# Performance work log

Measured on AMD Instinct MI355X. Metric: run time of the kernel, lower is better.

Reference implementation:

```python
import jax, jax.numpy as jnp
import numpy as np
from functools import partial

D = 1024
H = 4 * D
E = 8
K_TOP = 2
B, T = 4, 2048
NEG_INF = jnp.float32(-1e30)


def setup_inputs() -> dict:
    key = jax.random.key(0)
    ks = jax.random.split(key, 12)
    s = 0.02
    return {
        "x": jax.random.normal(ks[0], (B, T, D), jnp.float32),
        "noise": jax.random.normal(ks[1], (B, T, E), jnp.float32),
        "gate_w": jax.random.normal(ks[2], (E, D), jnp.float32) * s,
        "gate_b": jnp.zeros((E,), jnp.float32),
        "var_w": jax.random.normal(ks[3], (E, D), jnp.float32) * s,
        "var_b": jnp.zeros((E,), jnp.float32),
        "w1": jax.random.normal(ks[4], (E, H, D), jnp.float32) * s,
        "b1": jnp.zeros((E, H), jnp.float32),
        "w2": jax.random.normal(ks[5], (E, D, H), jnp.float32) * s,
        "b2": jnp.zeros((E, D), jnp.float32),
    }


def reference(x, noise, gate_w, gate_b, var_w, var_b, w1, b1, w2, b2):
    # Noisy top-k gating
    logits = jnp.einsum("btd,ed->bte", x, gate_w) + gate_b          # [B,T,E]
    std = jax.nn.softplus(jnp.einsum("btd,ed->bte", x, var_w) + var_b)
    noisy = logits + noise * std                                      # [B,T,E]
    _, idx = jax.lax.top_k(noisy, K_TOP)                              # [B,T,K]
    # boolean top-k mask over experts
    mask = (idx[..., None] == jnp.arange(E)).any(axis=-2)             # [B,T,E]
    coef = jax.nn.softmax(jnp.where(mask, noisy, NEG_INF), axis=-1)   # zeros outside top-k

    # Combine: sum_e coef_e * FFN_e(x). coef is exactly 0 for non-selected
    # experts, so this equals the masked gather/scatter math. Scan over the
    # small expert dim to avoid a [E,B,T,H] intermediate.
    coef_e = jnp.moveaxis(coef, -1, 0)                                # [E,B,T]

    def body(acc, ew):
        w1e, b1e, w2e, b2e, ce = ew
        h = jax.nn.relu(jnp.einsum("btd,hd->bth", x, w1e) + b1e)
        y = jnp.einsum("bth,dh->btd", h, w2e) + b2e
        return acc + y * ce[..., None], None

    out, _ = jax.lax.scan(body, jnp.zeros_like(x), (w1, b1, w2, b2, coef_e))
    return out
```

## Files before the change

### kernel.cpp

```cpp
#include <hip/hip_runtime.h>
#include <hip/hip_bf16.h>
#include <math.h>

#define NTOK 8192
#define DD   1024
#define HH   4096
#define NE   8
#define BM 256
#define BN 256
#define BK 64
#define SLOT_CAP (2 * NTOK + NE * BM)

typedef __bf16 bf16;
typedef __bf16 bf16x8 __attribute__((ext_vector_type(8)));
typedef __bf16 bf16x4 __attribute__((ext_vector_type(4)));
typedef float  f32x4  __attribute__((ext_vector_type(4)));

typedef __attribute__((address_space(3))) unsigned char lds_u8;
typedef const __attribute__((address_space(1))) unsigned char g_u8;

__device__ __forceinline__ void gload16(const bf16* g, bf16* l) {
  __builtin_amdgcn_global_load_lds((g_u8*)g, (lds_u8*)l, 16, 0, 0);
}

__device__ __forceinline__ float softplus_f(float v) {
  return fmaxf(v, 0.f) + log1pf(expf(-fabsf(v)));
}

__global__ __launch_bounds__(64) void moe_gate_kernel(
    const float* __restrict__ x, const float* __restrict__ noise,
    const float* __restrict__ gate_w, const float* __restrict__ gate_b,
    const float* __restrict__ var_w,  const float* __restrict__ var_b,
    float* __restrict__ coef2, int* __restrict__ t2e, int* __restrict__ counts)
{
  const int t = blockIdx.x;
  const int lane = threadIdx.x;
  const float* xt = x + (size_t)t * DD;
  float pg[NE], pv[NE];
  #pragma unroll
  for (int e = 0; e < NE; ++e) { pg[e] = 0.f; pv[e] = 0.f; }
  #pragma unroll 4
  for (int i = 0; i < DD / 64; ++i) {
    const int d = lane + i * 64;
    const float xv = xt[d];
    #pragma unroll
    for (int e = 0; e < NE; ++e) {
      pg[e] = fmaf(xv, gate_w[e * DD + d], pg[e]);
      pv[e] = fmaf(xv, var_w[e * DD + d], pv[e]);
    }
  }
  #pragma unroll
  for (int e = 0; e < NE; ++e) {
    #pragma unroll
    for (int off = 32; off; off >>= 1) {
      pg[e] += __shfl_xor(pg[e], off);
      pv[e] += __shfl_xor(pv[e], off);
    }
  }
  if (lane == 0) {
    float noisy[NE];
    #pragma unroll
    for (int e = 0; e < NE; ++e) {
      const float lg = pg[e] + gate_b[e];
      const float sd = softplus_f(pv[e] + var_b[e]);
      noisy[e] = lg + noise[t * NE + e] * sd;
    }
    int i1 = 0; float n1 = noisy[0];
    #pragma unroll
    for (int e = 1; e < NE; ++e) if (noisy[e] > n1) { n1 = noisy[e]; i1 = e; }
    int i2 = -1; float n2 = -3.0e38f;
    #pragma unroll
    for (int e = 0; e < NE; ++e) if (e != i1 && noisy[e] > n2) { n2 = noisy[e]; i2 = e; }
    const float e2 = expf(n2 - n1);
    const float den = 1.f + e2;
    coef2[t * 2 + 0] = 1.f / den;
    coef2[t * 2 + 1] = e2 / den;
    t2e[t * 2 + 0] = i1;
    t2e[t * 2 + 1] = i2;
    atomicAdd(&counts[i1], 1);
    atomicAdd(&counts[i2], 1);
  }
}

__global__ void moe_offsets_kernel(const int* __restrict__ counts, int* __restrict__ po) {
  if (threadIdx.x == 0) {
    int acc = 0;
    po[0] = 0;
    for (int e = 0; e < NE; ++e) {
      acc += ((counts[e] + BM - 1) / BM) * BM;
      po[e + 1] = acc;
    }
  }
}

__global__ __launch_bounds__(256) void moe_scatter_kernel(
    const int* __restrict__ t2e, const float* __restrict__ coef2,
    const int* __restrict__ po, int* __restrict__ cnt2,
    int* __restrict__ assign_tok, float* __restrict__ slot_coef)
{
  const int t = blockIdx.x * 256 + threadIdx.x;
  if (t >= NTOK) return;
  #pragma unroll
  for (int k = 0; k < 2; ++k) {
    const int e = t2e[t * 2 + k];
    const int pos = atomicAdd(&cnt2[e], 1);
    const int slot = po[e] + pos;
    assign_tok[slot] = t;
    slot_coef[slot] = coef2[t * 2 + k];
  }
}

__global__ __launch_bounds__(256) void cvt_bf16_kernel(const float* __restrict__ src,
                                                       bf16* __restrict__ dst, int n4) {
  for (int i = blockIdx.x * 256 + threadIdx.x; i < n4; i += gridDim.x * 256) {
    const float4 f = ((const float4*)src)[i];
    bf16x4 v;
    v[0] = (bf16)f.x; v[1] = (bf16)f.y; v[2] = (bf16)f.z; v[3] = (bf16)f.w;
    ((bf16x4*)dst)[i] = v;
  }
}

template<int KDIM, int NCOLS, bool FFN1>
__global__ __launch_bounds__(512, 2) void moe_gemm_kernel(
    const bf16* __restrict__ Asrc, const bf16* __restrict__ Wsrc,
    const float* __restrict__ bias,
    const int* __restrict__ assign_tok, const float* __restrict__ slot_coef,
    const int* __restrict__ po,
    bf16* __restrict__ hout, float* __restrict__ out,
    int chunk_base, int gx)
{
  __shared__ bf16 smA[2][BM * BK];
  __shared__ bf16 smB[2][BN * BK];
  __shared__ int toks[BM];

  const int nwg = gx * (NCOLS / BN);
  const int lin = blockIdx.x;
  const int q = nwg >> 3, r = nwg & 7;
  const int xcd = lin & 7, idx = lin >> 3;
  const int wg = (xcd < r ? xcd * (q + 1) : r * (q + 1) + (xcd - r) * q) + idx;
  const int bx = wg % gx, by = wg / gx;

  const int row0 = chunk_base + bx * BM;
  const int po8 = po[NE];
  if (row0 >= po8) return;
  int e = 0;
  while (row0 >= po[e + 1]) ++e;
  const int bn0 = by * BN;
  const bf16* We = Wsrc + (size_t)e * ((size_t)HH * DD);

  const int tid = threadIdx.x, lane = tid & 63;
  if (tid < BM) toks[tid] = assign_tok[row0 + tid];
  __syncthreads();

  const int t7 = tid & 7;
  const bf16* aptr[4];
  const bf16* bptr[4];
  #pragma unroll
  for (int i = 0; i < 4; ++i) {
    const int g = i * 512 + tid;
    const int row = g >> 3;
    const int c8 = ((t7 ^ (row & 7)) * 8);
    int ar;
    if constexpr (FFN1) {
      const int s = toks[row];
      ar = s < 0 ? 0 : s;
    } else {
      ar = row0 - chunk_base + row;
    }
    aptr[i] = Asrc + (size_t)ar * KDIM + c8;
    bptr[i] = We + (size_t)(bn0 + row) * KDIM + c8;
  }

  auto stage = [&](int sel, int k0) {
    #pragma unroll
    for (int i = 0; i < 4; ++i)
      gload16(aptr[i] + k0, &smA[sel][(i * 512 + tid) * 8]);
    #pragma unroll
    for (int i = 0; i < 4; ++i)
      gload16(bptr[i] + k0, &smB[sel][(i * 512 + tid) * 8]);
  };

  const int wid = tid >> 6, wr = wid >> 2, wc = wid & 3;
  const int la = lane & 15, hi = lane >> 4;
  f32x4 acc[8][4];
  #pragma unroll
  for (int m = 0; m < 8; ++m)
    #pragma unroll
    for (int n = 0; n < 4; ++n) acc[m][n] = {0.f, 0.f, 0.f, 0.f};

  constexpr int NK = KDIM / BK;
  stage(0, 0);
  __syncthreads();
  #pragma unroll 2
  for (int ks = 0; ks < NK; ++ks) {
    const int cur = ks & 1;
    if (ks + 1 < NK) stage(cur ^ 1, (ks + 1) * BK);
    const bf16* A = smA[cur];
    const bf16* B = smB[cur];
    #pragma unroll
    for (int kk = 0; kk < 2; ++kk) {
      bf16x8 af[8], bf_[4];
      #pragma unroll
      for (int m = 0; m < 8; ++m) {
        const int rw = wr * 128 + m * 16 + la;
        const int c8 = ((kk * 4 + hi) ^ (rw & 7)) * 8;
        af[m] = *(const bf16x8*)(A + rw * 64 + c8);
      }
      #pragma unroll
      for (int n = 0; n < 4; ++n) {
        const int rw = wc * 64 + n * 16 + la;
        const int c8 = ((kk * 4 + hi) ^ (rw & 7)) * 8;
        bf_[n] = *(const bf16x8*)(B + rw * 64 + c8);
      }
      #pragma unroll
      for (int m = 0; m < 8; ++m)
        #pragma unroll
        for (int n = 0; n < 4; ++n)
          acc[m][n] = __builtin_amdgcn_mfma_f32_16x16x32_bf16(af[m], bf_[n], acc[m][n], 0, 0, 0);
    }
    __syncthreads();
  }

  if constexpr (FFN1) {
    #pragma unroll
    for (int n = 0; n < 4; ++n) {
      const int col = bn0 + wc * 64 + n * 16 + la;
      const float bb = bias[e * NCOLS + col];
      #pragma unroll
      for (int m = 0; m < 8; ++m) {
        const int rl = wr * 128 + m * 16 + hi * 4;
        #pragma unroll
        for (int rr = 0; rr < 4; ++rr) {
          float v = acc[m][n][rr] + bb;
          v = v > 0.f ? v : 0.f;
          hout[(size_t)(row0 - chunk_base + rl + rr) * HH + col] = (bf16)v;
        }
      }
    }
  } else {
    #pragma unroll
    for (int n = 0; n < 4; ++n) {
      const int col = bn0 + wc * 64 + n * 16 + la;
      const float bb = bias[e * NCOLS + col];
      #pragma unroll
      for (int m = 0; m < 8; ++m) {
        const int rl = wr * 128 + m * 16 + hi * 4;
        #pragma unroll
        for (int rr = 0; rr < 4; ++rr) {
          const int tl = rl + rr;
          const int tok = toks[tl];
          if (tok >= 0) {
            const float c = slot_coef[row0 + tl];
            atomicAdd(out + (size_t)tok * DD + col, c * (acc[m][n][rr] + bb));
          }
        }
      }
    }
  }
}

extern "C" void kernel_launch(void* const* d_in, const int* in_sizes, int n_in,
                              void* d_out, int out_size, void* d_ws, size_t ws_size,
                              hipStream_t stream) {
  const float* x      = (const float*)d_in[0];
  const float* noise  = (const float*)d_in[1];
  const float* gate_w = (const float*)d_in[2];
  const float* gate_b = (const float*)d_in[3];
  const float* var_w  = (const float*)d_in[4];
  const float* var_b  = (const float*)d_in[5];
  const float* w1     = (const float*)d_in[6];
  const float* b1     = (const float*)d_in[7];
  const float* w2     = (const float*)d_in[8];
  const float* b2     = (const float*)d_in[9];
  float* out = (float*)d_out;
  (void)in_sizes; (void)n_in; (void)out_size;

  char* ws = (char*)d_ws;
  size_t off = 0;
  auto alloc = [&](size_t bytes) {
    off = (off + 255) & ~(size_t)255;
    size_t o = off;
    off += bytes;
    return o;
  };
  bf16*  xb         = (bf16*)(ws + alloc((size_t)NTOK * DD * 2));
  float* coef2      = (float*)(ws + alloc((size_t)NTOK * 2 * 4));
  int*   t2e        = (int*)(ws + alloc((size_t)NTOK * 2 * 4));
  int*   counts     = (int*)(ws + alloc(64));
  int*   cnt2       = counts + 8;
  int*   po         = (int*)(ws + alloc(64));
  int*   assign_tok = (int*)(ws + alloc((size_t)SLOT_CAP * 4));
  float* slot_coef  = (float*)(ws + alloc((size_t)SLOT_CAP * 4));
  bf16*  w1b        = (bf16*)(ws + alloc((size_t)NE * HH * DD * 2));
  bf16*  w2b        = (bf16*)(ws + alloc((size_t)NE * DD * HH * 2));
  off = (off + 255) & ~(size_t)255;
  const size_t h_avail = ws_size > off ? ws_size - off : 0;
  int chunk_rows = (int)(h_avail / ((size_t)HH * 2));
  chunk_rows = (chunk_rows / BM) * BM;
  if (chunk_rows < BM) chunk_rows = BM;
  if (chunk_rows > SLOT_CAP) chunk_rows = SLOT_CAP;
  bf16* hbuf = (bf16*)(ws + off);

  hipMemsetAsync(counts, 0, 64, stream);
  hipMemsetAsync(assign_tok, 0xFF, (size_t)SLOT_CAP * 4, stream);
  hipMemsetAsync(out, 0, (size_t)NTOK * DD * 4, stream);

  moe_gate_kernel<<<NTOK, 64, 0, stream>>>(x, noise, gate_w, gate_b, var_w, var_b,
                                           coef2, t2e, counts);
  moe_offsets_kernel<<<1, 64, 0, stream>>>(counts, po);
  moe_scatter_kernel<<<NTOK / 256, 256, 0, stream>>>(t2e, coef2, po, cnt2,
                                                     assign_tok, slot_coef);
  cvt_bf16_kernel<<<2048, 256, 0, stream>>>(x, xb, NTOK * DD / 4);
  cvt_bf16_kernel<<<2048, 256, 0, stream>>>(w1, w1b, NE * HH * DD / 4);
  cvt_bf16_kernel<<<2048, 256, 0, stream>>>(w2, w2b, NE * DD * HH / 4);

  const int rounds = (SLOT_CAP + chunk_rows - 1) / chunk_rows;
  for (int r = 0; r < rounds; ++r) {
    const int cb = r * chunk_rows;
    const int rows_here = (cb + chunk_rows <= SLOT_CAP) ? chunk_rows : (SLOT_CAP - cb);
    const int gx = rows_here / BM;
    moe_gemm_kernel<DD, HH, true><<<gx * (HH / BN), 512, 0, stream>>>(
        xb, w1b, b1, assign_tok, slot_coef, po, hbuf, nullptr, cb, gx);
    moe_gemm_kernel<HH, DD, false><<<gx * (DD / BN), 512, 0, stream>>>(
        hbuf, w2b, b2, assign_tok, slot_coef, po, nullptr, out, cb, gx);
  }
}
```

Baseline: 995.0 us.

## Rewrite MoE GEMM mainloop with 4-stage LDS pipeline and split-K FFN2

Replaces the double-buffered BK=64 mainloop with a four-deep ring of BK=32 stages, using manual vmcnt waits and raw barriers so global-to-LDS loads overlap MFMA work. MFMA bursts are wrapped in setprio, and A fragments are loaded in two halves to reduce register pressure. The second FFN GEMM is split along K into two z-slices that accumulate atomically, with only slice zero adding bias, to put more workgroups on the device. The change adds deeper pipelining and a new LDS swizzle, and doubles the atomic traffic on the output.

```diff
diff --git a/kernel.cpp b/kernel.cpp
--- a/kernel.cpp
+++ b/kernel.cpp
@@ -8,7 +8,6 @@
 #define NE   8
 #define BM 256
 #define BN 256
-#define BK 64
 #define SLOT_CAP (2 * NTOK + NE * BM)
 
 typedef __bf16 bf16;
@@ -120,8 +119,8 @@
   }
 }
 
-template<int KDIM, int NCOLS, bool FFN1>
-__global__ __launch_bounds__(512, 2) void moe_gemm_kernel(
+template<int KDIM, int KSTRIDE, int NCOLS, bool FFN1>
+__global__ __launch_bounds__(512, 2) void moe_gemm8_kernel(
     const bf16* __restrict__ Asrc, const bf16* __restrict__ Wsrc,
     const float* __restrict__ bias,
     const int* __restrict__ assign_tok, const float* __restrict__ slot_coef,
@@ -129,8 +128,10 @@
     bf16* __restrict__ hout, float* __restrict__ out,
     int chunk_base, int gx)
 {
-  __shared__ bf16 smA[2][BM * BK];
-  __shared__ bf16 smB[2][BN * BK];
+  constexpr int NI  = KDIM / 128;
+  constexpr int KHT = KDIM / 32;
+  __shared__ bf16 smA[32768];
+  __shared__ bf16 smB[32768];
   __shared__ int toks[BM];
 
   const int nwg = gx * (NCOLS / BN);
@@ -146,82 +147,88 @@
   int e = 0;
   while (row0 >= po[e + 1]) ++e;
   const int bn0 = by * BN;
-  const bf16* We = Wsrc + (size_t)e * ((size_t)HH * DD);
-
-  const int tid = threadIdx.x, lane = tid & 63;
+  const size_t kbase = (size_t)blockIdx.z * KDIM;
+  const bf16* We = Wsrc + (size_t)e * ((size_t)HH * DD) + kbase;
+  const bf16* As = Asrc + kbase;
+
+  const int tid = threadIdx.x, lane = tid & 63, wid = tid >> 6;
   if (tid < BM) toks[tid] = assign_tok[row0 + tid];
   __syncthreads();
 
-  const int t7 = tid & 7;
-  const bf16* aptr[4];
-  const bf16* bptr[4];
-  #pragma unroll
-  for (int i = 0; i < 4; ++i) {
-    const int g = i * 512 + tid;
-    const int row = g >> 3;
-    const int c8 = ((t7 ^ (row & 7)) * 8);
-    int ar;
-    if constexpr (FFN1) {
-      const int s = toks[row];
-      ar = s < 0 ? 0 : s;
-    } else {
-      ar = row0 - chunk_base + row;
-    }
-    aptr[i] = Asrc + (size_t)ar * KDIM + c8;
-    bptr[i] = We + (size_t)(bn0 + row) * KDIM + c8;
-  }
-
-  auto stage = [&](int sel, int k0) {
-    #pragma unroll
-    for (int i = 0; i < 4; ++i)
-      gload16(aptr[i] + k0, &smA[sel][(i * 512 + tid) * 8]);
-    #pragma unroll
-    for (int i = 0; i < 4; ++i)
-      gload16(bptr[i] + k0, &smB[sel][(i * 512 + tid) * 8]);
+  const int srcc = (((lane & 3) ^ ((lane >> 2) & 3)) * 8);
+  const int rt0 = wid * 16 + (lane >> 2);
+  const int rt1 = (8 + wid) * 16 + (lane >> 2);
+  int ar0, ar1;
+  if constexpr (FFN1) {
+    const int s0 = toks[rt0]; ar0 = s0 < 0 ? 0 : s0;
+    const int s1 = toks[rt1]; ar1 = s1 < 0 ? 0 : s1;
+  } else {
+    ar0 = row0 - chunk_base + rt0;
+    ar1 = row0 - chunk_base + rt1;
+  }
+  const bf16* ap0 = As + (size_t)ar0 * KSTRIDE + srcc;
+  const bf16* ap1 = As + (size_t)ar1 * KSTRIDE + srcc;
+  const bf16* bp0 = We + (size_t)(bn0 + rt0) * KSTRIDE + srcc;
+  const bf16* bp1 = We + (size_t)(bn0 + rt1) * KSTRIDE + srcc;
+
+  auto stage = [&](int rr, int kh) {
+    const int ko = kh * 32;
+    gload16(ap0 + ko, &smA[rr * 8192 + wid * 512]);
+    gload16(ap1 + ko, &smA[rr * 8192 + (8 + wid) * 512]);
+    gload16(bp0 + ko, &smB[rr * 8192 + wid * 512]);
+    gload16(bp1 + ko, &smB[rr * 8192 + (8 + wid) * 512]);
   };
 
-  const int wid = tid >> 6, wr = wid >> 2, wc = wid & 3;
+  const int wr = wid >> 2, wc = wid & 3;
   const int la = lane & 15, hi = lane >> 4;
+  const int cph = (hi ^ (la & 3)) * 8;
+  const int aBase = wr * 4096 + la * 32 + cph;
+  const int bBase = wc * 2048 + la * 32 + cph;
+
   f32x4 acc[8][4];
   #pragma unroll
   for (int m = 0; m < 8; ++m)
     #pragma unroll
     for (int n = 0; n < 4; ++n) acc[m][n] = {0.f, 0.f, 0.f, 0.f};
 
-  constexpr int NK = KDIM / BK;
-  stage(0, 0);
-  __syncthreads();
-  #pragma unroll 2
-  for (int ks = 0; ks < NK; ++ks) {
-    const int cur = ks & 1;
-    if (ks + 1 < NK) stage(cur ^ 1, (ks + 1) * BK);
-    const bf16* A = smA[cur];
-    const bf16* B = smB[cur];
-    #pragma unroll
-    for (int kk = 0; kk < 2; ++kk) {
-      bf16x8 af[8], bf_[4];
-      #pragma unroll
-      for (int m = 0; m < 8; ++m) {
-        const int rw = wr * 128 + m * 16 + la;
-        const int c8 = ((kk * 4 + hi) ^ (rw & 7)) * 8;
-        af[m] = *(const bf16x8*)(A + rw * 64 + c8);
-      }
-      #pragma unroll
-      for (int n = 0; n < 4; ++n) {
-        const int rw = wc * 64 + n * 16 + la;
-        const int c8 = ((kk * 4 + hi) ^ (rw & 7)) * 8;
-        bf_[n] = *(const bf16x8*)(B + rw * 64 + c8);
-      }
-      #pragma unroll
-      for (int m = 0; m < 8; ++m)
+  stage(0, 0); stage(1, 1); stage(2, 2);
+
+  for (int i = 0; i < NI; ++i) {
+    #pragma unroll
+    for (int pp = 0; pp < 4; ++pp) {
+      asm volatile("s_waitcnt vmcnt(8)" ::: "memory");
+      asm volatile("s_barrier" ::: "memory");
+      bf16x8 a0[4], bb[4];
+      #pragma unroll
+      for (int m = 0; m < 4; ++m)
+        a0[m] = *(const bf16x8*)(&smA[pp * 8192 + aBase + m * 512]);
+      #pragma unroll
+      for (int n = 0; n < 4; ++n)
+        bb[n] = *(const bf16x8*)(&smB[pp * 8192 + bBase + n * 512]);
+      stage((pp + 3) & 3, (i * 4 + 3 + pp) & (KHT - 1));
+      __builtin_amdgcn_s_setprio(1);
+      #pragma unroll
+      for (int m = 0; m < 4; ++m)
         #pragma unroll
         for (int n = 0; n < 4; ++n)
-          acc[m][n] = __builtin_amdgcn_mfma_f32_16x16x32_bf16(af[m], bf_[n], acc[m][n], 0, 0, 0);
-    }
-    __syncthreads();
+          acc[m][n] = __builtin_amdgcn_mfma_f32_16x16x32_bf16(a0[m], bb[n], acc[m][n], 0, 0, 0);
+      __builtin_amdgcn_s_setprio(0);
+      bf16x8 a1[4];
+      #pragma unroll
+      for (int m = 0; m < 4; ++m)
+        a1[m] = *(const bf16x8*)(&smA[pp * 8192 + aBase + (4 + m) * 512]);
+      __builtin_amdgcn_s_setprio(1);
+      #pragma unroll
+      for (int m = 0; m < 4; ++m)
+        #pragma unroll
+        for (int n = 0; n < 4; ++n)
+          acc[4 + m][n] = __builtin_amdgcn_mfma_f32_16x16x32_bf16(a1[m], bb[n], acc[4 + m][n], 0, 0, 0);
+      __builtin_amdgcn_s_setprio(0);
+    }
   }
 
   if constexpr (FFN1) {
+    const int hrow0 = row0 - chunk_base;
     #pragma unroll
     for (int n = 0; n < 4; ++n) {
       const int col = bn0 + wc * 64 + n * 16 + la;
@@ -233,15 +240,16 @@
         for (int rr = 0; rr < 4; ++rr) {
           float v = acc[m][n][rr] + bb;
           v = v > 0.f ? v : 0.f;
-          hout[(size_t)(row0 - chunk_base + rl + rr) * HH + col] = (bf16)v;
+          hout[(size_t)(hrow0 + rl + rr) * HH + col] = (bf16)v;
         }
       }
     }
   } else {
+    const bool addb = (blockIdx.z == 0);
     #pragma unroll
     for (int n = 0; n < 4; ++n) {
       const int col = bn0 + wc * 64 + n * 16 + la;
-      const float bb = bias[e * NCOLS + col];
+      const float bb = addb ? bias[e * NCOLS + col] : 0.f;
       #pragma unroll
       for (int m = 0; m < 8; ++m) {
         const int rl = wr * 128 + m * 16 + hi * 4;
@@ -319,9 +327,11 @@
     const int cb = r * chunk_rows;
     const int rows_here = (cb + chunk_rows <= SLOT_CAP) ? chunk_rows : (SLOT_CAP - cb);
     const int gx = rows_here / BM;
-    moe_gemm_kernel<DD, HH, true><<<gx * (HH / BN), 512, 0, stream>>>(
+    dim3 g1(gx * (HH / BN), 1, 1);
+    moe_gemm8_kernel<DD, DD, HH, true><<<g1, 512, 0, stream>>>(
         xb, w1b, b1, assign_tok, slot_coef, po, hbuf, nullptr, cb, gx);
-    moe_gemm_kernel<HH, DD, false><<<gx * (DD / BN), 512, 0, stream>>>(
+    dim3 g2(gx * (DD / BN), 1, 2);
+    moe_gemm8_kernel<HH / 2, HH, DD, false><<<g2, 512, 0, stream>>>(
         hbuf, w2b, b2, assign_tok, slot_coef, po, nullptr, out, cb, gx);
   }
 }
```

Measured after the change: 952.5 us. -4.3%, faster.
